# Optimization experiments

Hardware: AMD Instinct MI355X
Metric: run time of the kernel (lower is better)

Reference implementation:

```python
import jax, jax.numpy as jnp
import numpy as np

BATCH = 4096
DIM = 2048
TEMPERATURE = 0.5


def setup_inputs() -> dict:
    key = jax.random.key(0)
    k1, k2 = jax.random.split(key)
    c_i = jax.random.normal(k1, (BATCH, DIM), dtype=jnp.float32)
    c_j = jax.random.normal(k2, (BATCH, DIM), dtype=jnp.float32)
    return {"c_i": c_i, "c_j": c_j}


def reference(c_i, c_j):
    # Original torch loop computes, for each i,j:
    #   kl[i, j] = sum_k softmax(c_j[j])_k * (log_softmax(c_j[j])_k - log_softmax(c_i[i])_k)
    #   logits = -kl / T ; loss = CE(logits, arange(B), reduction='sum') / B
    # Fused: kl = hneg[None, :] - Li @ Q.T where hneg[j] = sum_k Q[j]*logQ[j].
    B = c_i.shape[0]
    Li = jax.nn.log_softmax(c_i, axis=-1)          # [B, D]
    LQ = jax.nn.log_softmax(c_j, axis=-1)          # [B, D]
    Q = jnp.exp(LQ)                                # softmax(c_j)
    hneg = jnp.sum(Q * LQ, axis=-1)                # [B] negative entropy of each c_j row
    cross = jnp.einsum("id,jd->ij", Li, Q)         # [B, B] sum_k Li[i,k]*Q[j,k]
    kl = hneg[None, :] - cross                     # [B, B]
    logits = -kl / TEMPERATURE
    logp = jax.nn.log_softmax(logits, axis=-1)     # [B, B]
    loss = -jnp.sum(jnp.diagonal(logp)) / B        # CE(sum) / batch_size
    return loss
```

## Files before the change

### kernel.cpp

```cpp
#include <hip/hip_runtime.h>
#include <hip/hip_bf16.h>
#include <math.h>

#define BATCH 4096
#define DIM   2048
#define INV_T 2.0f

#define BM 256
#define BN 256

typedef float floatx4 __attribute__((ext_vector_type(4)));
typedef int   intx4   __attribute__((ext_vector_type(4)));
typedef int   intx8   __attribute__((ext_vector_type(8)));

static __device__ __forceinline__ void gld_lds16(const void* g, void* l) {
  __builtin_amdgcn_global_load_lds(
      (const __attribute__((address_space(1))) void*)g,
      (__attribute__((address_space(3))) void*)l, 16, 0, 0);
}

static __device__ __forceinline__ intx8 comb8(intx4 lo, intx4 hi) {
  intx8 r;
  r[0] = lo[0]; r[1] = lo[1]; r[2] = lo[2]; r[3] = lo[3];
  r[4] = hi[0]; r[5] = hi[1]; r[6] = hi[2]; r[7] = hi[3];
  return r;
}

__global__ __launch_bounds__(256) void prep_kernel(
    const float* __restrict__ ci, const float* __restrict__ cj,
    unsigned char* __restrict__ Li8, unsigned char* __restrict__ Qb8,
    float* __restrict__ hneg, float* __restrict__ isc,
    float* __restrict__ rowsum, float* __restrict__ out)
{
  const int lane = threadIdx.x & 63;
  const int wave = threadIdx.x >> 6;
  const int row = blockIdx.x * 4 + wave;
  const bool isj = row >= BATCH;
  const int r = isj ? row - BATCH : row;
  const float* __restrict__ src = (isj ? cj : ci) + (size_t)r * DIM;

  float v[32];
  #pragma unroll
  for (int i = 0; i < 8; ++i) {
    float4 t = ((const float4*)src)[i * 64 + lane];
    v[i * 4 + 0] = t.x; v[i * 4 + 1] = t.y;
    v[i * 4 + 2] = t.z; v[i * 4 + 3] = t.w;
  }

  float m = v[0];
  #pragma unroll
  for (int i = 1; i < 32; ++i) m = fmaxf(m, v[i]);
  #pragma unroll
  for (int off = 32; off >= 1; off >>= 1) m = fmaxf(m, __shfl_xor(m, off));

  float s = 0.f;
  #pragma unroll
  for (int i = 0; i < 32; ++i) s += __expf(v[i] - m);
  #pragma unroll
  for (int off = 32; off >= 1; off >>= 1) s += __shfl_xor(s, off);
  const float ls = m + __logf(s);

  float scale = 1.f;
  int t = 0;
  if (isj) {
    const float qmax = __expf(m - ls);
    const int be = (int)((__float_as_uint(qmax) >> 23) & 0xff);
    t = 134 - be;
    scale = __uint_as_float((unsigned)(t + 127) << 23);
  }

  unsigned char* dst = (isj ? Qb8 : Li8) + (size_t)r * DIM;
  float h = 0.f;
  #pragma unroll
  for (int i = 0; i < 8; ++i) {
    float f[4];
    #pragma unroll
    for (int j = 0; j < 4; ++j) {
      const float li = v[i * 4 + j] - ls;
      if (isj) {
        const float q = __expf(li);
        h += q * li;
        f[j] = q * scale;
      } else {
        f[j] = li;
      }
    }
    int w = __builtin_amdgcn_cvt_pk_fp8_f32(f[0], f[1], 0, false);
    w = __builtin_amdgcn_cvt_pk_fp8_f32(f[2], f[3], w, true);
    ((int*)dst)[i * 64 + lane] = w;
  }

  if (isj) {
    #pragma unroll
    for (int off = 32; off >= 1; off >>= 1) h += __shfl_xor(h, off);
    if (lane == 0) {
      hneg[r] = h;
      isc[r] = __uint_as_float((unsigned)(127 - t) << 23);
      rowsum[r] = 0.f;
    }
  }
  if (row == 0 && lane == 0) out[0] = 0.f;
}

__global__ __launch_bounds__(512, 1) void gemm_lse_kernel(
    const unsigned char* __restrict__ Li8, const unsigned char* __restrict__ Qb8,
    const float* __restrict__ hneg, const float* __restrict__ isc,
    float* __restrict__ rowsum, float* __restrict__ diag)
{
  __shared__ __attribute__((aligned(16))) unsigned char As_[2][BM * 128];
  __shared__ __attribute__((aligned(16))) unsigned char Bs_[2][BN * 128];

  const int tid  = threadIdx.x;
  const int lin = blockIdx.x;
  const int xc  = lin & 7;
  const int sq  = lin >> 3;
  const int by  = (xc & 3) * 4 + (sq & 3);
  const int bx  = (xc >> 2) * 8 + (sq >> 2);

  const int lane = tid & 63;
  const int wave = tid >> 6;
  const int wm   = wave >> 2;
  const int wn   = wave & 3;

  int soff[4];
  #pragma unroll
  for (int s = 0; s < 4; ++s) {
    const int p = tid + 512 * s;
    const int row = p >> 3;
    const int cbg = (p & 7) ^ (row & 7);
    soff[s] = row * DIM + cbg * 16;
  }
  const unsigned char* Abase = Li8 + (size_t)(by * BM) * DIM;
  const unsigned char* Bbase = Qb8 + (size_t)(bx * BN) * DIM;

  const int rl = lane & 15;
  const int q  = lane >> 4;
  const int sw = rl & 7;

  floatx4 acc[8][4];
  const floatx4 z = {0.f, 0.f, 0.f, 0.f};
  #pragma unroll
  for (int mt = 0; mt < 8; ++mt)
    #pragma unroll
    for (int nt = 0; nt < 4; ++nt) acc[mt][nt] = z;

  #pragma unroll
  for (int s = 0; s < 4; ++s) {
    gld_lds16(Abase + soff[s], &As_[0][0] + (tid + 512 * s) * 16);
    gld_lds16(Bbase + soff[s], &Bs_[0][0] + (tid + 512 * s) * 16);
  }

  for (int t = 0; t < 16; ++t) {
    const int cur = t & 1;
    const unsigned char* Ab = &As_[cur][0];
    const unsigned char* Bb = &Bs_[cur][0];
    unsigned char* An = &As_[cur ^ 1][0];
    unsigned char* Bn = &Bs_[cur ^ 1][0];
    const int kn = (t + 1) * 128;

    if (t < 15) {
      #pragma unroll
      for (int s = 0; s < 4; ++s) {
        gld_lds16(Abase + soff[s] + kn, An + (tid + 512 * s) * 16);
        gld_lds16(Bbase + soff[s] + kn, Bn + (tid + 512 * s) * 16);
      }
      asm volatile("s_waitcnt vmcnt(8)" ::: "memory");
    } else {
      asm volatile("s_waitcnt vmcnt(0)" ::: "memory");
    }
    asm volatile("s_barrier" ::: "memory");

    intx8 bf[4];
    #pragma unroll
    for (int nt = 0; nt < 4; ++nt) {
      const int rb = wn * 64 + nt * 16 + rl;
      const int q0 = rb * 8 + ((2 * q) ^ sw);
      const int q1 = rb * 8 + ((2 * q + 1) ^ sw);
      bf[nt] = comb8(*(const intx4*)(Bb + q0 * 16),
                     *(const intx4*)(Bb + q1 * 16));
    }
    intx8 af[2];
    {
      const int ra = wm * 128 + rl;
      const int a0 = ra * 8 + ((2 * q) ^ sw);
      const int a1 = ra * 8 + ((2 * q + 1) ^ sw);
      af[0] = comb8(*(const intx4*)(Ab + a0 * 16),
                    *(const intx4*)(Ab + a1 * 16));
    }
    #pragma unroll
    for (int s = 0; s < 8; ++s) {
      if (s < 7) {
        const int ra = wm * 128 + (s + 1) * 16 + rl;
        const int a0 = ra * 8 + ((2 * q) ^ sw);
        const int a1 = ra * 8 + ((2 * q + 1) ^ sw);
        af[(s + 1) & 1] = comb8(*(const intx4*)(Ab + a0 * 16),
                                *(const intx4*)(Ab + a1 * 16));
      }
      __builtin_amdgcn_s_setprio(1);
      #pragma unroll
      for (int nt = 0; nt < 4; ++nt)
        acc[s][nt] = __builtin_amdgcn_mfma_scale_f32_16x16x128_f8f6f4(
            af[s & 1], bf[nt], acc[s][nt],
            0, 0,
            0, 127,
            0, 127);
      __builtin_amdgcn_s_setprio(0);
    }

    asm volatile("s_barrier" ::: "memory");
  }

  const int col0 = bx * BN + wn * 64 + rl;
  float hn[4], sc[4];
  #pragma unroll
  for (int nt = 0; nt < 4; ++nt) {
    hn[nt] = hneg[col0 + nt * 16];
    sc[nt] = isc[col0 + nt * 16];
  }
  const int row0 = by * BM + wm * 128 + (q << 2);

  if (bx == by && wm == (wn >> 1) && q == (rl >> 2)) {
    #pragma unroll
    for (int half = 0; half < 2; ++half) {
      #pragma unroll
      for (int nt = 0; nt < 4; ++nt) {
        #pragma unroll
        for (int rr = 0; rr < 4; ++rr) {
          if ((wn & 1) == half && (rl & 3) == rr)
            diag[bx * BN + wn * 64 + nt * 16 + rl] =
                acc[half * 4 + nt][nt][rr] * sc[nt];
        }
      }
    }
  }

  #pragma unroll
  for (int mt = 0; mt < 8; ++mt) {
    #pragma unroll
    for (int rr = 0; rr < 4; ++rr) {
      float p = 0.f;
      #pragma unroll
      for (int nt = 0; nt < 4; ++nt)
        p += __expf(INV_T * (acc[mt][nt][rr] * sc[nt] - hn[nt]));
      p += __shfl_xor(p, 1);
      p += __shfl_xor(p, 2);
      p += __shfl_xor(p, 4);
      p += __shfl_xor(p, 8);
      if (rl == 0)
        atomicAdd(&rowsum[row0 + mt * 16 + rr], p);
    }
  }
}

__global__ __launch_bounds__(256) void finalize_kernel(
    const float* __restrict__ hneg, const float* __restrict__ rowsum,
    const float* __restrict__ diag, float* __restrict__ out)
{
  const int i = blockIdx.x * 256 + threadIdx.x;
  const int lane = threadIdx.x & 63;
  const int wave = threadIdx.x >> 6;

  float c = __logf(rowsum[i]) - INV_T * (diag[i] - hneg[i]);
  #pragma unroll
  for (int off = 32; off >= 1; off >>= 1) c += __shfl_xor(c, off);

  __shared__ float red[4];
  if (lane == 0) red[wave] = c;
  __syncthreads();
  if (threadIdx.x == 0)
    atomicAdd(out, (red[0] + red[1] + red[2] + red[3]) * (1.0f / BATCH));
}

extern "C" void kernel_launch(void* const* d_in, const int* in_sizes, int n_in,
                              void* d_out, int out_size, void* d_ws, size_t ws_size,
                              hipStream_t stream) {
  const float* ci = (const float*)d_in[0];
  const float* cj = (const float*)d_in[1];
  float* out = (float*)d_out;

  unsigned char* Li8 = (unsigned char*)d_ws;
  unsigned char* Qb8 = Li8 + (size_t)BATCH * DIM;
  float* hneg   = (float*)(Qb8 + (size_t)BATCH * DIM);
  float* isc    = hneg + BATCH;
  float* rowsum = isc + BATCH;
  float* diag   = rowsum + BATCH;

  prep_kernel<<<2 * BATCH / 4, 256, 0, stream>>>(ci, cj, Li8, Qb8, hneg, isc, rowsum, out);
  gemm_lse_kernel<<<(BATCH / BM) * (BATCH / BN), 512, 0, stream>>>(Li8, Qb8, hneg, isc, rowsum, diag);
  finalize_kernel<<<BATCH / 256, 256, 0, stream>>>(hneg, rowsum, diag, out);
}
```

Baseline: 142.8 us.

## Pre-swizzle Q into MFMA fragment layout and load B directly to registers

The prep kernel now writes the fp8 Q matrix in a layout that matches the MFMA B-fragment order, so each wave can fetch its B operands straight from global memory into registers. The B shared-memory tile and its LDS reads are removed, and B fragments are double-buffered in registers alongside the existing A LDS pipeline. This halves LDS footprint and LDS read traffic, but B loads are now per-wave global loads with no reuse across waves in the block (wm=0 and wm=1 fetch the same data), which relies on cache hits and adds latency exposure.

```diff
diff --git a/kernel.cpp b/kernel.cpp
--- a/kernel.cpp
+++ b/kernel.cpp
@@ -87,7 +87,13 @@
     }
     int w = __builtin_amdgcn_cvt_pk_fp8_f32(f[0], f[1], 0, false);
     w = __builtin_amdgcn_cvt_pk_fp8_f32(f[2], f[3], w, true);
-    ((int*)dst)[i * 64 + lane] = w;
+    if (isj) {
+      const int idx = ((r >> 4) << 13) | ((i * 2 + (lane >> 5)) << 9)
+                    | (((lane >> 3) & 3) << 7) | ((r & 15) << 3) | (lane & 7);
+      ((int*)Qb8)[idx] = w;
+    } else {
+      ((int*)dst)[i * 64 + lane] = w;
+    }
   }
 
   if (isj) {
@@ -108,7 +114,6 @@
     float* __restrict__ rowsum, float* __restrict__ diag)
 {
   __shared__ __attribute__((aligned(16))) unsigned char As_[2][BM * 128];
-  __shared__ __attribute__((aligned(16))) unsigned char Bs_[2][BN * 128];
 
   const int tid  = threadIdx.x;
   const int lin = blockIdx.x;
@@ -131,7 +136,8 @@
     soff[s] = row * DIM + cbg * 16;
   }
   const unsigned char* Abase = Li8 + (size_t)(by * BM) * DIM;
-  const unsigned char* Bbase = Qb8 + (size_t)(bx * BN) * DIM;
+  const unsigned char* Bfbase =
+      Qb8 + (size_t)(bx * 16 + wn * 4) * 32768 + lane * 32;
 
   const int rl = lane & 15;
   const int q  = lane >> 4;
@@ -145,70 +151,69 @@
     for (int nt = 0; nt < 4; ++nt) acc[mt][nt] = z;
 
   #pragma unroll
-  for (int s = 0; s < 4; ++s) {
+  for (int s = 0; s < 4; ++s)
     gld_lds16(Abase + soff[s], &As_[0][0] + (tid + 512 * s) * 16);
-    gld_lds16(Bbase + soff[s], &Bs_[0][0] + (tid + 512 * s) * 16);
-  }
-
-  for (int t = 0; t < 16; ++t) {
-    const int cur = t & 1;
-    const unsigned char* Ab = &As_[cur][0];
-    const unsigned char* Bb = &Bs_[cur][0];
-    unsigned char* An = &As_[cur ^ 1][0];
-    unsigned char* Bn = &Bs_[cur ^ 1][0];
-    const int kn = (t + 1) * 128;
-
-    if (t < 15) {
-      #pragma unroll
-      for (int s = 0; s < 4; ++s) {
-        gld_lds16(Abase + soff[s] + kn, An + (tid + 512 * s) * 16);
-        gld_lds16(Bbase + soff[s] + kn, Bn + (tid + 512 * s) * 16);
-      }
-      asm volatile("s_waitcnt vmcnt(8)" ::: "memory");
-    } else {
-      asm volatile("s_waitcnt vmcnt(0)" ::: "memory");
-    }
-    asm volatile("s_barrier" ::: "memory");
-
-    intx8 bf[4];
-    #pragma unroll
-    for (int nt = 0; nt < 4; ++nt) {
-      const int rb = wn * 64 + nt * 16 + rl;
-      const int q0 = rb * 8 + ((2 * q) ^ sw);
-      const int q1 = rb * 8 + ((2 * q + 1) ^ sw);
-      bf[nt] = comb8(*(const intx4*)(Bb + q0 * 16),
-                     *(const intx4*)(Bb + q1 * 16));
-    }
-    intx8 af[2];
-    {
-      const int ra = wm * 128 + rl;
-      const int a0 = ra * 8 + ((2 * q) ^ sw);
-      const int a1 = ra * 8 + ((2 * q + 1) ^ sw);
-      af[0] = comb8(*(const intx4*)(Ab + a0 * 16),
-                    *(const intx4*)(Ab + a1 * 16));
-    }
-    #pragma unroll
-    for (int s = 0; s < 8; ++s) {
-      if (s < 7) {
-        const int ra = wm * 128 + (s + 1) * 16 + rl;
-        const int a0 = ra * 8 + ((2 * q) ^ sw);
-        const int a1 = ra * 8 + ((2 * q + 1) ^ sw);
-        af[(s + 1) & 1] = comb8(*(const intx4*)(Ab + a0 * 16),
-                                *(const intx4*)(Ab + a1 * 16));
-      }
-      __builtin_amdgcn_s_setprio(1);
-      #pragma unroll
-      for (int nt = 0; nt < 4; ++nt)
-        acc[s][nt] = __builtin_amdgcn_mfma_scale_f32_16x16x128_f8f6f4(
-            af[s & 1], bf[nt], acc[s][nt],
-            0, 0,
-            0, 127,
-            0, 127);
-      __builtin_amdgcn_s_setprio(0);
-    }
-
-    asm volatile("s_barrier" ::: "memory");
-  }
+  intx8 bfA[4], bfB[4];
+  #pragma unroll
+  for (int nt = 0; nt < 4; ++nt)
+    bfA[nt] = comb8(*(const intx4*)(Bfbase + nt * 32768),
+                    *(const intx4*)(Bfbase + nt * 32768 + 16));
+
+#define KTILE(T, CUR, bfU, bfN)                                               \
+  {                                                                           \
+    const int t_ = (T);                                                       \
+    const unsigned char* Ab = &As_[CUR][0];                                   \
+    if (t_ < 15) {                                                            \
+      unsigned char* An = &As_[(CUR) ^ 1][0];                                 \
+      const int kn = (t_ + 1) * 128;                                          \
+      _Pragma("unroll")                                                       \
+      for (int s = 0; s < 4; ++s)                                             \
+        gld_lds16(Abase + soff[s] + kn, An + (tid + 512 * s) * 16);           \
+      _Pragma("unroll")                                                       \
+      for (int nt = 0; nt < 4; ++nt)                                          \
+        bfN[nt] = comb8(                                                      \
+            *(const intx4*)(Bfbase + nt * 32768 + (t_ + 1) * 2048),           \
+            *(const intx4*)(Bfbase + nt * 32768 + (t_ + 1) * 2048 + 16));     \
+      asm volatile("s_waitcnt vmcnt(12)" ::: "memory");                       \
+    } else {                                                                  \
+      asm volatile("s_waitcnt vmcnt(0)" ::: "memory");                        \
+    }                                                                         \
+    asm volatile("s_barrier" ::: "memory");                                   \
+    intx8 af[2];                                                              \
+    {                                                                         \
+      const int ra = wm * 128 + rl;                                           \
+      const int a0 = ra * 8 + ((2 * q) ^ sw);                                 \
+      const int a1 = ra * 8 + ((2 * q + 1) ^ sw);                             \
+      af[0] = comb8(*(const intx4*)(Ab + a0 * 16),                            \
+                    *(const intx4*)(Ab + a1 * 16));                           \
+    }                                                                         \
+    _Pragma("unroll")                                                         \
+    for (int s = 0; s < 8; ++s) {                                             \
+      if (s < 7) {                                                            \
+        const int ra = wm * 128 + (s + 1) * 16 + rl;                          \
+        const int a0 = ra * 8 + ((2 * q) ^ sw);                               \
+        const int a1 = ra * 8 + ((2 * q + 1) ^ sw);                           \
+        af[(s + 1) & 1] = comb8(*(const intx4*)(Ab + a0 * 16),                \
+                                *(const intx4*)(Ab + a1 * 16));               \
+      }                                                                       \
+      __builtin_amdgcn_s_setprio(1);                                          \
+      _Pragma("unroll")                                                       \
+      for (int nt = 0; nt < 4; ++nt)                                          \
+        acc[s][nt] = __builtin_amdgcn_mfma_scale_f32_16x16x128_f8f6f4(        \
+            af[s & 1], bfU[nt], acc[s][nt],                                   \
+            0, 0,                     \
+            0, 127,                                         \
+            0, 127);                                        \
+      __builtin_amdgcn_s_setprio(0);                                          \
+    }                                                                         \
+    asm volatile("s_barrier" ::: "memory");                                   \
+  }
+
+  for (int tt = 0; tt < 8; ++tt) {
+    KTILE(2 * tt,     0, bfA, bfB);
+    KTILE(2 * tt + 1, 1, bfB, bfA);
+  }
+#undef KTILE
 
   const int col0 = bx * BN + wn * 64 + rl;
   float hn[4], sc[4];
```

Measured after the change: 166.6 us. 16.6% more time.

## Use 16 waves per GEMM block and reuse softmax exponentials in prep

Applied to the files above, without the earlier changes.

The GEMM+LSE kernel now runs 1024 threads (16 waves in a 4x4 grid, each owning a 64x64 subtile) instead of 512 threads with 128x64 subtiles. This halves per-wave accumulators and per-thread async load counts, giving more waves to hide LDS and MFMA latency. The cost is more LDS fragment reads, since B fragments are now loaded by twice as many waves, and the A prefetch double-buffering inside the k-step is dropped. In prep, the exponentials from the sum pass are kept and reused for q, replacing a second exp with a multiply by the reciprocal sum.

```diff
diff --git a/kernel.cpp b/kernel.cpp
--- a/kernel.cpp
+++ b/kernel.cpp
@@ -53,17 +53,19 @@
   #pragma unroll
   for (int off = 32; off >= 1; off >>= 1) m = fmaxf(m, __shfl_xor(m, off));
 
+  float e[32];
   float s = 0.f;
   #pragma unroll
-  for (int i = 0; i < 32; ++i) s += __expf(v[i] - m);
+  for (int i = 0; i < 32; ++i) { e[i] = __expf(v[i] - m); s += e[i]; }
   #pragma unroll
   for (int off = 32; off >= 1; off >>= 1) s += __shfl_xor(s, off);
   const float ls = m + __logf(s);
+  const float inv_s = 1.0f / s;
 
   float scale = 1.f;
   int t = 0;
   if (isj) {
-    const float qmax = __expf(m - ls);
+    const float qmax = inv_s;
     const int be = (int)((__float_as_uint(qmax) >> 23) & 0xff);
     t = 134 - be;
     scale = __uint_as_float((unsigned)(t + 127) << 23);
@@ -78,7 +80,7 @@
     for (int j = 0; j < 4; ++j) {
       const float li = v[i * 4 + j] - ls;
       if (isj) {
-        const float q = __expf(li);
+        const float q = e[i * 4 + j] * inv_s;
         h += q * li;
         f[j] = q * scale;
       } else {
@@ -102,7 +104,7 @@
   if (row == 0 && lane == 0) out[0] = 0.f;
 }
 
-__global__ __launch_bounds__(512, 1) void gemm_lse_kernel(
+__global__ __launch_bounds__(1024, 1) void gemm_lse_kernel(
     const unsigned char* __restrict__ Li8, const unsigned char* __restrict__ Qb8,
     const float* __restrict__ hneg, const float* __restrict__ isc,
     float* __restrict__ rowsum, float* __restrict__ diag)
@@ -119,13 +121,13 @@
 
   const int lane = tid & 63;
   const int wave = tid >> 6;
-  const int wm   = wave >> 2;
-  const int wn   = wave & 3;
-
-  int soff[4];
-  #pragma unroll
-  for (int s = 0; s < 4; ++s) {
-    const int p = tid + 512 * s;
+  const int ww   = wave >> 2;
+  const int wc   = wave & 3;
+
+  int soff[2];
+  #pragma unroll
+  for (int s = 0; s < 2; ++s) {
+    const int p = tid + 1024 * s;
     const int row = p >> 3;
     const int cbg = (p & 7) ^ (row & 7);
     soff[s] = row * DIM + cbg * 16;
@@ -137,34 +139,34 @@
   const int q  = lane >> 4;
   const int sw = rl & 7;
 
-  floatx4 acc[8][4];
+  floatx4 acc[4][4];
   const floatx4 z = {0.f, 0.f, 0.f, 0.f};
   #pragma unroll
-  for (int mt = 0; mt < 8; ++mt)
+  for (int mt = 0; mt < 4; ++mt)
     #pragma unroll
     for (int nt = 0; nt < 4; ++nt) acc[mt][nt] = z;
 
   #pragma unroll
-  for (int s = 0; s < 4; ++s) {
-    gld_lds16(Abase + soff[s], &As_[0][0] + (tid + 512 * s) * 16);
-    gld_lds16(Bbase + soff[s], &Bs_[0][0] + (tid + 512 * s) * 16);
+  for (int s = 0; s < 2; ++s) {
+    gld_lds16(Abase + soff[s], &As_[0][0] + (tid + 1024 * s) * 16);
+    gld_lds16(Bbase + soff[s], &Bs_[0][0] + (tid + 1024 * s) * 16);
   }
 
   for (int t = 0; t < 16; ++t) {
     const int cur = t & 1;
     const unsigned char* Ab = &As_[cur][0];
     const unsigned char* Bb = &Bs_[cur][0];
-    unsigned char* An = &As_[cur ^ 1][0];
-    unsigned char* Bn = &Bs_[cur ^ 1][0];
-    const int kn = (t + 1) * 128;
 
     if (t < 15) {
-      #pragma unroll
-      for (int s = 0; s < 4; ++s) {
-        gld_lds16(Abase + soff[s] + kn, An + (tid + 512 * s) * 16);
-        gld_lds16(Bbase + soff[s] + kn, Bn + (tid + 512 * s) * 16);
+      unsigned char* An = &As_[cur ^ 1][0];
+      unsigned char* Bn = &Bs_[cur ^ 1][0];
+      const int kn = (t + 1) * 128;
+      #pragma unroll
+      for (int s = 0; s < 2; ++s) {
+        gld_lds16(Abase + soff[s] + kn, An + (tid + 1024 * s) * 16);
+        gld_lds16(Bbase + soff[s] + kn, Bn + (tid + 1024 * s) * 16);
       }
-      asm volatile("s_waitcnt vmcnt(8)" ::: "memory");
+      asm volatile("s_waitcnt vmcnt(4)" ::: "memory");
     } else {
       asm volatile("s_waitcnt vmcnt(0)" ::: "memory");
     }
@@ -173,34 +175,24 @@
     intx8 bf[4];
     #pragma unroll
     for (int nt = 0; nt < 4; ++nt) {
-      const int rb = wn * 64 + nt * 16 + rl;
+      const int rb = wc * 64 + nt * 16 + rl;
       const int q0 = rb * 8 + ((2 * q) ^ sw);
       const int q1 = rb * 8 + ((2 * q + 1) ^ sw);
       bf[nt] = comb8(*(const intx4*)(Bb + q0 * 16),
                      *(const intx4*)(Bb + q1 * 16));
     }
-    intx8 af[2];
-    {
-      const int ra = wm * 128 + rl;
+    #pragma unroll
+    for (int mt = 0; mt < 4; ++mt) {
+      const int ra = ww * 64 + mt * 16 + rl;
       const int a0 = ra * 8 + ((2 * q) ^ sw);
       const int a1 = ra * 8 + ((2 * q + 1) ^ sw);
-      af[0] = comb8(*(const intx4*)(Ab + a0 * 16),
-                    *(const intx4*)(Ab + a1 * 16));
-    }
-    #pragma unroll
-    for (int s = 0; s < 8; ++s) {
-      if (s < 7) {
-        const int ra = wm * 128 + (s + 1) * 16 + rl;
-        const int a0 = ra * 8 + ((2 * q) ^ sw);
-        const int a1 = ra * 8 + ((2 * q + 1) ^ sw);
-        af[(s + 1) & 1] = comb8(*(const intx4*)(Ab + a0 * 16),
-                                *(const intx4*)(Ab + a1 * 16));
-      }
+      const intx8 af = comb8(*(const intx4*)(Ab + a0 * 16),
+                             *(const intx4*)(Ab + a1 * 16));
       __builtin_amdgcn_s_setprio(1);
       #pragma unroll
       for (int nt = 0; nt < 4; ++nt)
-        acc[s][nt] = __builtin_amdgcn_mfma_scale_f32_16x16x128_f8f6f4(
-            af[s & 1], bf[nt], acc[s][nt],
+        acc[mt][nt] = __builtin_amdgcn_mfma_scale_f32_16x16x128_f8f6f4(
+            af, bf[nt], acc[mt][nt],
             0, 0,
             0, 127,
             0, 127);
@@ -210,32 +202,28 @@
     asm volatile("s_barrier" ::: "memory");
   }
 
-  const int col0 = bx * BN + wn * 64 + rl;
+  const int col0 = bx * BN + wc * 64 + rl;
   float hn[4], sc[4];
   #pragma unroll
   for (int nt = 0; nt < 4; ++nt) {
     hn[nt] = hneg[col0 + nt * 16];
     sc[nt] = isc[col0 + nt * 16];
   }
-  const int row0 = by * BM + wm * 128 + (q << 2);
-
-  if (bx == by && wm == (wn >> 1) && q == (rl >> 2)) {
-    #pragma unroll
-    for (int half = 0; half < 2; ++half) {
-      #pragma unroll
-      for (int nt = 0; nt < 4; ++nt) {
-        #pragma unroll
-        for (int rr = 0; rr < 4; ++rr) {
-          if ((wn & 1) == half && (rl & 3) == rr)
-            diag[bx * BN + wn * 64 + nt * 16 + rl] =
-                acc[half * 4 + nt][nt][rr] * sc[nt];
-        }
+  const int row0 = by * BM + ww * 64 + (q << 2);
+
+  if (bx == by && ww == wc && q == (rl >> 2)) {
+    #pragma unroll
+    for (int nt = 0; nt < 4; ++nt) {
+      #pragma unroll
+      for (int rr = 0; rr < 4; ++rr) {
+        if ((rl & 3) == rr)
+          diag[bx * BN + wc * 64 + nt * 16 + rl] = acc[nt][nt][rr] * sc[nt];
       }
     }
   }
 
   #pragma unroll
-  for (int mt = 0; mt < 8; ++mt) {
+  for (int mt = 0; mt < 4; ++mt) {
     #pragma unroll
     for (int rr = 0; rr < 4; ++rr) {
       float p = 0.f;
@@ -286,6 +274,6 @@
   float* diag   = rowsum + BATCH;
 
   prep_kernel<<<2 * BATCH / 4, 256, 0, stream>>>(ci, cj, Li8, Qb8, hneg, isc, rowsum, out);
-  gemm_lse_kernel<<<(BATCH / BM) * (BATCH / BN), 512, 0, stream>>>(Li8, Qb8, hneg, isc, rowsum, diag);
+  gemm_lse_kernel<<<(BATCH / BM) * (BATCH / BN), 1024, 0, stream>>>(Li8, Qb8, hneg, isc, rowsum, diag);
   finalize_kernel<<<BATCH / 256, 256, 0, stream>>>(hneg, rowsum, diag, out);
 }
```

Measured after the change: 232.5 us. 62.8% more time.

## Fuse finalize into GEMM via last-block counter and reuse softmax exponentials

Applied to the files above, without the earlier changes.

Removes the separate finalize kernel. The GEMM kernel now keeps a global atomic counter, and the last block to finish reduces rowsum, diag and hneg into the output, which saves one launch. The prep kernel also keeps the exponentials from the sum pass and multiplies by the reciprocal of the sum instead of calling exp a second time. It derives the fp8 scale exponent from 1/s instead of qmax. Diagonal writes now use atomicExch so they are visible to the last block. The cost is a serialized tail reduction in one block and extra register pressure in prep.

```diff
diff --git a/kernel.cpp b/kernel.cpp
--- a/kernel.cpp
+++ b/kernel.cpp
@@ -30,7 +30,7 @@
     const float* __restrict__ ci, const float* __restrict__ cj,
     unsigned char* __restrict__ Li8, unsigned char* __restrict__ Qb8,
     float* __restrict__ hneg, float* __restrict__ isc,
-    float* __restrict__ rowsum, float* __restrict__ out)
+    float* __restrict__ rowsum, unsigned* __restrict__ cnt)
 {
   const int lane = threadIdx.x & 63;
   const int wave = threadIdx.x >> 6;
@@ -53,18 +53,19 @@
   #pragma unroll
   for (int off = 32; off >= 1; off >>= 1) m = fmaxf(m, __shfl_xor(m, off));
 
+  float e[32];
   float s = 0.f;
   #pragma unroll
-  for (int i = 0; i < 32; ++i) s += __expf(v[i] - m);
+  for (int i = 0; i < 32; ++i) { e[i] = __expf(v[i] - m); s += e[i]; }
   #pragma unroll
   for (int off = 32; off >= 1; off >>= 1) s += __shfl_xor(s, off);
   const float ls = m + __logf(s);
+  const float inv_s = 1.0f / s;
 
   float scale = 1.f;
   int t = 0;
   if (isj) {
-    const float qmax = __expf(m - ls);
-    const int be = (int)((__float_as_uint(qmax) >> 23) & 0xff);
+    const int be = (int)((__float_as_uint(inv_s) >> 23) & 0xff);
     t = 134 - be;
     scale = __uint_as_float((unsigned)(t + 127) << 23);
   }
@@ -78,7 +79,7 @@
     for (int j = 0; j < 4; ++j) {
       const float li = v[i * 4 + j] - ls;
       if (isj) {
-        const float q = __expf(li);
+        const float q = e[i * 4 + j] * inv_s;
         h += q * li;
         f[j] = q * scale;
       } else {
@@ -99,13 +100,14 @@
       rowsum[r] = 0.f;
     }
   }
-  if (row == 0 && lane == 0) out[0] = 0.f;
+  if (row == 0 && lane == 0) cnt[0] = 0u;
 }
 
 __global__ __launch_bounds__(512, 1) void gemm_lse_kernel(
     const unsigned char* __restrict__ Li8, const unsigned char* __restrict__ Qb8,
     const float* __restrict__ hneg, const float* __restrict__ isc,
-    float* __restrict__ rowsum, float* __restrict__ diag)
+    float* __restrict__ rowsum, float* __restrict__ diag,
+    unsigned* __restrict__ cnt, float* __restrict__ out)
 {
   __shared__ __attribute__((aligned(16))) unsigned char As_[2][BM * 128];
   __shared__ __attribute__((aligned(16))) unsigned char Bs_[2][BN * 128];
@@ -154,11 +156,11 @@
     const int cur = t & 1;
     const unsigned char* Ab = &As_[cur][0];
     const unsigned char* Bb = &Bs_[cur][0];
-    unsigned char* An = &As_[cur ^ 1][0];
-    unsigned char* Bn = &Bs_[cur ^ 1][0];
-    const int kn = (t + 1) * 128;
 
     if (t < 15) {
+      unsigned char* An = &As_[cur ^ 1][0];
+      unsigned char* Bn = &Bs_[cur ^ 1][0];
+      const int kn = (t + 1) * 128;
       #pragma unroll
       for (int s = 0; s < 4; ++s) {
         gld_lds16(Abase + soff[s] + kn, An + (tid + 512 * s) * 16);
@@ -227,8 +229,8 @@
         #pragma unroll
         for (int rr = 0; rr < 4; ++rr) {
           if ((wn & 1) == half && (rl & 3) == rr)
-            diag[bx * BN + wn * 64 + nt * 16 + rl] =
-                acc[half * 4 + nt][nt][rr] * sc[nt];
+            atomicExch(&diag[bx * BN + wn * 64 + nt * 16 + rl],
+                       acc[half * 4 + nt][nt][rr] * sc[nt]);
         }
       }
     }
@@ -250,25 +252,33 @@
         atomicAdd(&rowsum[row0 + mt * 16 + rr], p);
     }
   }
-}
-
-__global__ __launch_bounds__(256) void finalize_kernel(
-    const float* __restrict__ hneg, const float* __restrict__ rowsum,
-    const float* __restrict__ diag, float* __restrict__ out)
-{
-  const int i = blockIdx.x * 256 + threadIdx.x;
-  const int lane = threadIdx.x & 63;
-  const int wave = threadIdx.x >> 6;
-
-  float c = __logf(rowsum[i]) - INV_T * (diag[i] - hneg[i]);
-  #pragma unroll
-  for (int off = 32; off >= 1; off >>= 1) c += __shfl_xor(c, off);
-
-  __shared__ float red[4];
-  if (lane == 0) red[wave] = c;
+
+  __shared__ unsigned last_flag;
   __syncthreads();
-  if (threadIdx.x == 0)
-    atomicAdd(out, (red[0] + red[1] + red[2] + red[3]) * (1.0f / BATCH));
+  if (tid == 0) {
+    __threadfence();
+    last_flag = (atomicAdd(cnt, 1u) == 255u);
+  }
+  __syncthreads();
+  if (last_flag) {
+    float c = 0.f;
+    #pragma unroll
+    for (int j = 0; j < 8; ++j) {
+      const int i = tid + j * 512;
+      c += __logf(rowsum[i]) - INV_T * (diag[i] - hneg[i]);
+    }
+    #pragma unroll
+    for (int off = 32; off >= 1; off >>= 1) c += __shfl_xor(c, off);
+    __shared__ float red[8];
+    if (lane == 0) red[wave] = c;
+    __syncthreads();
+    if (tid == 0) {
+      float tot = 0.f;
+      #pragma unroll
+      for (int w = 0; w < 8; ++w) tot += red[w];
+      out[0] = tot * (1.0f / BATCH);
+    }
+  }
 }
 
 extern "C" void kernel_launch(void* const* d_in, const int* in_sizes, int n_in,
@@ -284,8 +294,9 @@
   float* isc    = hneg + BATCH;
   float* rowsum = isc + BATCH;
   float* diag   = rowsum + BATCH;
-
-  prep_kernel<<<2 * BATCH / 4, 256, 0, stream>>>(ci, cj, Li8, Qb8, hneg, isc, rowsum, out);
-  gemm_lse_kernel<<<(BATCH / BM) * (BATCH / BN), 512, 0, stream>>>(Li8, Qb8, hneg, isc, rowsum, diag);
-  finalize_kernel<<<BATCH / 256, 256, 0, stream>>>(hneg, rowsum, diag, out);
-}
+  unsigned* cnt = (unsigned*)(diag + BATCH);
+
+  prep_kernel<<<2 * BATCH / 4, 256, 0, stream>>>(ci, cj, Li8, Qb8, hneg, isc, rowsum, cnt);
+  gemm_lse_kernel<<<(BATCH / BM) * (BATCH / BN), 512, 0, stream>>>(
+      Li8, Qb8, hneg, isc, rowsum, diag, cnt, out);
+}
```

New measurement: 143.3 us. No clear change (+0.3%).
